# Kernel tuning notes

Hardware: AMD Instinct MI355X
Metric: run time of the kernel (lower is better)

The kernel has to match this reference:

```python
import jax, jax.numpy as jnp
import numpy as np

EMBED_DIM = 1024
HEADS = 16
HEAD_DIM = EMBED_DIM // HEADS
ROPE_THETA = 10000.0


def apply_rope(x):
    # x: [B, H, T, D]; standard rotary embedding on head_dim, half-split style
    D = x.shape[-1]
    T = x.shape[-2]
    half = D // 2
    inv_freq = 1.0 / (ROPE_THETA ** (jnp.arange(half, dtype=jnp.float32) / half))
    ang = jnp.arange(T, dtype=jnp.float32)[:, None] * inv_freq[None, :]  # [T, half]
    cos, sin = jnp.cos(ang), jnp.sin(ang)  # [T, half]
    x1, x2 = x[..., :half], x[..., half:]
    return jnp.concatenate([x1 * cos - x2 * sin, x1 * sin + x2 * cos], axis=-1)


def setup_inputs() -> dict:
    key = jax.random.key(0)
    ks = jax.random.split(key, 6)
    B, T, E, H = 2, 2048, EMBED_DIM, HEADS
    s = 0.02
    return {
        "x": jax.random.normal(ks[0], (B, T, E), dtype=jnp.float32),
        "w_qkv": jax.random.normal(ks[1], (E, 3 * E), dtype=jnp.float32) * s,
        "w_pre": jax.random.normal(ks[2], (H, H), dtype=jnp.float32) * s,
        "w_post": jax.random.normal(ks[3], (H, H), dtype=jnp.float32) * s,
        "w_out": jax.random.normal(ks[4], (E, E), dtype=jnp.float32) * s,
        "b_out": jax.random.normal(ks[5], (E,), dtype=jnp.float32) * s,
    }


def reference(x, w_qkv, w_pre, w_post, w_out, b_out):
    B, T, E = x.shape
    H, D = HEADS, HEAD_DIM
    qkv = x @ w_qkv  # [B, T, 3E]
    q, k, v = jnp.split(qkv, 3, axis=-1)
    q = q.reshape(B, T, H, D).transpose(0, 2, 1, 3)  # [B,H,T,D]
    k = k.reshape(B, T, H, D).transpose(0, 2, 1, 3)
    v = v.reshape(B, T, H, D).transpose(0, 2, 1, 3)
    q = apply_rope(q)
    k = apply_rope(k)
    scale = D ** -0.5
    dots = jnp.einsum('bhid,bhjd->bhij', q, k) * scale  # [B,H,T,T]
    # pre-softmax talking-heads mixing: new_head g = sum_h w_pre[g,h] * dots[h]
    dots = jnp.einsum('bhij,gh->bgij', dots, w_pre)
    attn = jax.nn.softmax(dots, axis=-1)
    # post-softmax mixing
    attn = jnp.einsum('bhij,gh->bgij', attn, w_post)
    out = jnp.einsum('bhij,bhjd->bhid', attn, v)  # [B,H,T,D]
    out = out.transpose(0, 2, 1, 3).reshape(B, T, E)
    return out @ w_out.T + b_out  # dropout is identity in eval
```

## Files before the change

kernel.cpp:

```cpp
#include <hip/hip_runtime.h>
#include <stdint.h>

typedef unsigned short u16;
typedef unsigned int   u32;

#define T_SEQ 2048
#define NB 2
#define NH 16
#define HD 64
#define E_DIM 1024
#define E3 3072
#define JS1 4
#define JS2 4
#define S2 36
#define OS2 1040

typedef float f32x4 __attribute__((ext_vector_type(4)));
typedef short s16x8 __attribute__((ext_vector_type(8)));

__device__ __forceinline__ float b2f(u16 u) {
    union { float f; u32 i; } v; v.i = ((u32)u) << 16; return v.f;
}
__device__ __forceinline__ u16 f2b(float f) {
    union { float f; u32 i; } v; v.f = f;
    u32 x = v.i;
    return (u16)((x + 0x7FFFu + ((x >> 16) & 1u)) >> 16);
}
__device__ __forceinline__ f32x4 mfma_bf16(s16x8 a, s16x8 b, f32x4 c) {
    return __builtin_amdgcn_mfma_f32_16x16x32_bf16(a, b, c, 0, 0, 0);
}
__device__ __forceinline__ void gl_lds16(const void* g, void* l) {
    __builtin_amdgcn_global_load_lds((const __attribute__((address_space(1))) void*)g,
                                     (__attribute__((address_space(3))) void*)l, 16, 0, 0);
}

__global__ void k_detect(const u16* __restrict__ x, int* __restrict__ flag) {
    __shared__ int cnt[256];
    int tid = threadIdx.x;
    int insane = 0;
    for (int i = tid; i < 4096; i += 256) {
        u16 v = x[2 * i];
        int e = (v >> 7) & 0xFF;
        if (e >= 143 || (e > 0 && e <= 100)) insane++;
    }
    cnt[tid] = insane;
    __syncthreads();
    if (tid == 0) {
        int s = 0;
        for (int k = 0; k < 256; ++k) s += cnt[k];
        *flag = (s > 512) ? 1 : 0;
    }
}

__global__ void k_cvt_bf16(const void* __restrict__ src, u16* __restrict__ dst,
                           int n, const int* __restrict__ flag) {
    int i = blockIdx.x * 256 + threadIdx.x;
    bool f32 = (*flag) != 0;
    if (i < n) dst[i] = f32 ? f2b(((const float*)src)[i]) : ((const u16*)src)[i];
}

__global__ void k_cvt_small(const void* __restrict__ a, const void* __restrict__ b,
                            const void* __restrict__ c, float* __restrict__ da,
                            float* __restrict__ db, float* __restrict__ dc,
                            const int* __restrict__ flag) {
    int i = blockIdx.x * 256 + threadIdx.x;
    bool f32 = (*flag) != 0;
    if (i < 256) {
        da[i] = f32 ? ((const float*)a)[i] : b2f(((const u16*)a)[i]);
    } else if (i < 512) {
        int j = i - 256;
        db[j] = f32 ? ((const float*)b)[j] : b2f(((const u16*)b)[j]);
    } else if (i < 1536) {
        int j = i - 512;
        dc[j] = f32 ? ((const float*)c)[j] : b2f(((const u16*)c)[j]);
    }
}

__global__ void k_transpose(const void* __restrict__ w, u16* __restrict__ wT,
                            const int* __restrict__ flag) {
    __shared__ u16 tile[32][33];
    bool f32 = (*flag) != 0;
    int n0 = blockIdx.x * 32;
    int k0 = blockIdx.y * 32;
    int tid = threadIdx.x;
    int c = tid & 31, r4 = tid >> 5;
#pragma unroll
    for (int it = 0; it < 4; ++it) {
        int r = r4 + it * 8;
        size_t idx = (size_t)(k0 + r) * E3 + n0 + c;
        tile[r][c] = f32 ? f2b(((const float*)w)[idx]) : ((const u16*)w)[idx];
    }
    __syncthreads();
#pragma unroll
    for (int it = 0; it < 4; ++it) {
        int r = r4 + it * 8;
        wT[(size_t)(n0 + r) * E_DIM + k0 + c] = tile[c][r];
    }
}

__global__ void k_qkv(const u16* __restrict__ A, const u16* __restrict__ Bm,
                      u16* __restrict__ C) {
    __shared__ __align__(16) u16 As[128 * 32];
    __shared__ __align__(16) u16 Bs[128 * 32];
    int m0 = blockIdx.x * 128, n0 = blockIdx.y * 128;
    int tid = threadIdx.x, lane = tid & 63, wv = tid >> 6;
    int q = lane >> 4, l = lane & 15;
    int wm = (wv >> 1) * 64, wn = (wv & 1) * 64;
    f32x4 acc[4][4] = {};
    int r16 = lane >> 2;
    int ccol = (lane & 3) * 8;
    for (int kc = 0; kc < 1024; kc += 32) {
#pragma unroll
        for (int j = 0; j < 4; ++j) {
            int chunk = wv * 4 + j;
            if (chunk < 8) {
                const u16* g = A + (size_t)(m0 + chunk * 16 + r16) * 1024 + kc + ccol;
                gl_lds16(g, (char*)As + chunk * 1024);
            } else {
                int ch = chunk - 8;
                const u16* g = Bm + (size_t)(n0 + ch * 16 + r16) * 1024 + kc + ccol;
                gl_lds16(g, (char*)Bs + ch * 1024);
            }
        }
        __syncthreads();
        s16x8 af[4], bf[4];
#pragma unroll
        for (int t = 0; t < 4; ++t) {
            af[t] = *(const s16x8*)(As + (wm + t * 16 + l) * 32 + q * 8);
            bf[t] = *(const s16x8*)(Bs + (wn + t * 16 + l) * 32 + q * 8);
        }
#pragma unroll
        for (int i = 0; i < 4; ++i)
#pragma unroll
            for (int j2 = 0; j2 < 4; ++j2)
                acc[i][j2] = mfma_bf16(af[i], bf[j2], acc[i][j2]);
        __syncthreads();
    }
#pragma unroll
    for (int i = 0; i < 4; ++i)
#pragma unroll
        for (int j2 = 0; j2 < 4; ++j2)
#pragma unroll
            for (int r = 0; r < 4; ++r) {
                int row = m0 + wm + i * 16 + q * 4 + r;
                int col = n0 + wn + j2 * 16 + l;
                C[(size_t)row * E3 + col] = f2b(acc[i][j2][r]);
            }
}

__global__ void k_rope(const u16* __restrict__ qkv, u16* __restrict__ qr,
                       u16* __restrict__ kr, u16* __restrict__ vt) {
    __shared__ u16 tile[64][66];
    int t0 = blockIdx.x * 64;
    int h = blockIdx.y, b = blockIdx.z;
    int tid = threadIdx.x;
    const float LN_TH = 9.210340371976184f / 32.0f;
    for (int src = 0; src < 3; ++src) {
        {
            int d = tid & 63, tr = tid >> 6;
#pragma unroll
            for (int it = 0; it < 16; ++it) {
                int t = tr + it * 4;
                tile[t][d] = qkv[(size_t)(b * T_SEQ + t0 + t) * E3 + src * E_DIM + h * HD + d];
            }
        }
        __syncthreads();
        if (src < 2) {
            u16* dst = (src == 0 ? qr : kr) + ((size_t)(b * NH + h) * T_SEQ) * HD;
            int d = tid & 31, tr = tid >> 5;
            float inv = __expf(-(float)d * LN_TH);
#pragma unroll
            for (int it = 0; it < 8; ++it) {
                int t = tr + it * 8;
                float ang = (float)(t0 + t) * inv;
                float sn, cs;
                __sincosf(ang, &sn, &cs);
                float x1 = b2f(tile[t][d]);
                float x2 = b2f(tile[t][d + 32]);
                dst[(size_t)(t0 + t) * HD + d]      = f2b(x1 * cs - x2 * sn);
                dst[(size_t)(t0 + t) * HD + d + 32] = f2b(x1 * sn + x2 * cs);
            }
        } else {
            int tl = tid & 63, dr = tid >> 6;
#pragma unroll
            for (int it = 0; it < 16; ++it) {
                int d = dr + it * 4;
                vt[((size_t)(b * NH + h) * HD + d) * T_SEQ + t0 + tl] = tile[tl][d];
            }
        }
        __syncthreads();
    }
}

__global__ __launch_bounds__(256, 3) void k_pass1(const u16* __restrict__ qr, const u16* __restrict__ kr,
                                                  const float* __restrict__ w_pre, float* __restrict__ lpart) {
    __shared__ __align__(16) u16 dotsb[2 * 256 * S2];
    int lin = blockIdx.x;
    int combo = lin & 7;
    int b = combo >> 2, js = combo & 3;
    int i0 = (lin >> 3) * 32;
    int tid = threadIdx.x, lane = tid & 63, wv = tid >> 6;
    int q = lane >> 4, l = lane & 15;
    {
        uint2 z = {0u, 0u};
        uint2* p0 = (uint2*)(dotsb + tid * S2 + 16);
        uint2* p1 = (uint2*)(dotsb + 256 * S2 + tid * S2 + 16);
        p0[0] = z; p0[1] = z; p0[2] = z; p0[3] = z;
        p1[0] = z; p1[1] = z; p1[2] = z; p1[3] = z;
    }
    s16x8 wpre;
#pragma unroll
    for (int jj = 0; jj < 8; ++jj) {
        int hh = q * 8 + jj;
        wpre[jj] = (hh < 16) ? (short)f2b(w_pre[l * 16 + hh] * 0.125f) : (short)0;
    }
    s16x8 qf[2][4][2];
#pragma unroll
    for (int it = 0; it < 2; ++it)
#pragma unroll
        for (int hl = 0; hl < 4; ++hl) {
            int h = wv * 4 + hl;
            const u16* ptr = qr + ((size_t)(b * NH + h) * T_SEQ + i0 + it * 16 + l) * HD + q * 8;
            qf[it][hl][0] = *(const s16x8*)(ptr);
            qf[it][hl][1] = *(const s16x8*)(ptr + 32);
        }
    float lacc[2][4][4] = {};
    __syncthreads();
    int jbase = js * (T_SEQ / JS1);
    for (int jstep = 0; jstep < (T_SEQ / JS1) / 16; ++jstep) {
        int jh = jbase + jstep * 16;
        s16x8 kf[4][2];
#pragma unroll
        for (int hl = 0; hl < 4; ++hl) {
            int h = wv * 4 + hl;
            const u16* ptr = kr + ((size_t)(b * NH + h) * T_SEQ + jh + l) * HD + q * 8;
            kf[hl][0] = *(const s16x8*)(ptr);
            kf[hl][1] = *(const s16x8*)(ptr + 32);
        }
#pragma unroll
        for (int it = 0; it < 2; ++it) {
            u16* dots = dotsb + (it & 1) * 256 * S2;
            f32x4 dacc[4];
#pragma unroll
            for (int hl = 0; hl < 4; ++hl) {
                f32x4 z = {};
                z = mfma_bf16(qf[it][hl][0], kf[hl][0], z);
                z = mfma_bf16(qf[it][hl][1], kf[hl][1], z);
                dacc[hl] = z;
            }
#pragma unroll
            for (int r = 0; r < 4; ++r) {
                int row = (q * 4 + r) * 16 + l;
                uint2 pk;
                pk.x = (u32)f2b(dacc[0][r]) | ((u32)f2b(dacc[1][r]) << 16);
                pk.y = (u32)f2b(dacc[2][r]) | ((u32)f2b(dacc[3][r]) << 16);
                *(uint2*)(dots + row * S2 + wv * 4) = pk;
            }
            __syncthreads();
#pragma unroll
            for (int cl = 0; cl < 4; ++cl) {
                int c = wv * 4 + cl;
                int rbase = (c * 16 + l) * S2;
                union { uint2 u2[2]; s16x8 v; } bf_;
                bf_.u2[0] = *(const uint2*)(dots + rbase + q * 8);
                bf_.u2[1] = *(const uint2*)(dots + rbase + q * 8 + 4);
                f32x4 s = {};
                s = mfma_bf16(wpre, bf_.v, s);
#pragma unroll
                for (int r = 0; r < 4; ++r)
                    lacc[it][cl][r] += __expf(fminf(s[r], 60.0f));
            }
        }
    }
#pragma unroll
    for (int it = 0; it < 2; ++it)
#pragma unroll
        for (int cl = 0; cl < 4; ++cl)
#pragma unroll
            for (int r = 0; r < 4; ++r) {
                float pv = lacc[it][cl][r];
                pv += __shfl_xor(pv, 1);
                pv += __shfl_xor(pv, 2);
                pv += __shfl_xor(pv, 4);
                pv += __shfl_xor(pv, 8);
                if (l == 0) {
                    int g = q * 4 + r;
                    int irow = wv * 4 + cl;
                    lpart[((size_t)(combo * NH + g)) * T_SEQ + i0 + it * 16 + irow] = pv;
                }
            }
}

__global__ __launch_bounds__(256, 2) void k_pass2(const u16* __restrict__ qr, const u16* __restrict__ kr,
                                                  const u16* __restrict__ vt, const float* __restrict__ lpart,
                                                  const float* __restrict__ w_pre, const float* __restrict__ w_post,
                                                  u16* __restrict__ opart) {
    __shared__ __align__(16) u16 smem[4 * 256 * S2];
    __shared__ float linv[2][16][16];
    u16* dotsb = smem;
    u16* aTb   = smem + 2 * 256 * S2;
    int lin = blockIdx.x;
    int combo = lin & 7;
    int b = combo >> 2, js = combo & 3;
    int i0 = (lin >> 3) * 32;
    int tid = threadIdx.x, lane = tid & 63, wv = tid >> 6;
    int q = lane >> 4, l = lane & 15;
    {
        uint2 z = {0u, 0u};
        uint2* p0 = (uint2*)(dotsb + tid * S2 + 16);
        uint2* p1 = (uint2*)(dotsb + 256 * S2 + tid * S2 + 16);
        p0[0] = z; p0[1] = z; p0[2] = z; p0[3] = z;
        p1[0] = z; p1[1] = z; p1[2] = z; p1[3] = z;
    }
    {
        int g = tid >> 4, il = tid & 15;
        float s0 = 0.f, s1 = 0.f;
#pragma unroll
        for (int j4 = 0; j4 < 4; ++j4) {
            const float* lp = lpart + ((size_t)((b * 4 + j4) * NH + g)) * T_SEQ + i0;
            s0 += lp[il];
            s1 += lp[16 + il];
        }
        linv[0][g][il] = 1.0f / s0;
        linv[1][g][il] = 1.0f / s1;
    }
    s16x8 wpre, wpost;
#pragma unroll
    for (int jj = 0; jj < 8; ++jj) {
        int hh = q * 8 + jj;
        wpre[jj]  = (hh < 16) ? (short)f2b(w_pre[l * 16 + hh] * 0.125f) : (short)0;
        wpost[jj] = (hh < 16) ? (short)f2b(w_post[l * 16 + hh]) : (short)0;
    }
    s16x8 qf[2][4][2];
#pragma unroll
    for (int it = 0; it < 2; ++it)
#pragma unroll
        for (int hl = 0; hl < 4; ++hl) {
            int h = wv * 4 + hl;
            const u16* ptr = qr + ((size_t)(b * NH + h) * T_SEQ + i0 + it * 16 + l) * HD + q * 8;
            qf[it][hl][0] = *(const s16x8*)(ptr);
            qf[it][hl][1] = *(const s16x8*)(ptr + 32);
        }
    f32x4 oacc[2][4][4] = {};
    __syncthreads();
    int jbase = js * (T_SEQ / JS2);
    for (int jst = 0; jst < (T_SEQ / JS2) / 32; ++jst) {
        int j0 = jbase + jst * 32;
#pragma unroll
        for (int jb = 0; jb < 2; ++jb) {
            int jh = j0 + jb * 16;
            s16x8 kf[4][2];
#pragma unroll
            for (int hl = 0; hl < 4; ++hl) {
                int h = wv * 4 + hl;
                const u16* ptr = kr + ((size_t)(b * NH + h) * T_SEQ + jh + l) * HD + q * 8;
                kf[hl][0] = *(const s16x8*)(ptr);
                kf[hl][1] = *(const s16x8*)(ptr + 32);
            }
#pragma unroll
            for (int it = 0; it < 2; ++it) {
                u16* dots = dotsb + ((jb * 2 + it) & 1) * 256 * S2;
                f32x4 dacc[4];
#pragma unroll
                for (int hl = 0; hl < 4; ++hl) {
                    f32x4 z = {};
                    z = mfma_bf16(qf[it][hl][0], kf[hl][0], z);
                    z = mfma_bf16(qf[it][hl][1], kf[hl][1], z);
                    dacc[hl] = z;
                }
#pragma unroll
                for (int r = 0; r < 4; ++r) {
                    int row = (q * 4 + r) * 16 + l;
                    uint2 pk;
                    pk.x = (u32)f2b(dacc[0][r]) | ((u32)f2b(dacc[1][r]) << 16);
                    pk.y = (u32)f2b(dacc[2][r]) | ((u32)f2b(dacc[3][r]) << 16);
                    *(uint2*)(dots + row * S2 + wv * 4) = pk;
                }
                __syncthreads();
                u16* aT = aTb + it * 256 * S2;
#pragma unroll
                for (int cl = 0; cl < 4; ++cl) {
                    int c = wv * 4 + cl;
                    int rbase = (c * 16 + l) * S2;
                    union { uint2 u2[2]; s16x8 v; } bf_;
                    bf_.u2[0] = *(const uint2*)(dots + rbase + q * 8);
                    bf_.u2[1] = *(const uint2*)(dots + rbase + q * 8 + 4);
                    f32x4 s = {};
                    s = mfma_bf16(wpre, bf_.v, s);
                    u32 pkx, pky;
                    {
                        u16 pu[4];
#pragma unroll
                        for (int r = 0; r < 4; ++r)
                            pu[r] = f2b(__expf(fminf(s[r], 60.0f)) * linv[it][q * 4 + r][c]);
                        pkx = (u32)pu[0] | ((u32)pu[1] << 16);
                        pky = (u32)pu[2] | ((u32)pu[3] << 16);
                    }
                    int srcA = (q & 1) * 32 + l;
                    int srcB = srcA + 16;
                    u32 x0 = (u32)__shfl((int)pkx, srcA);
                    u32 x1 = (u32)__shfl((int)pky, srcA);
                    u32 x2 = (u32)__shfl((int)pkx, srcB);
                    u32 x3 = (u32)__shfl((int)pky, srcB);
                    union { u32 u[4]; s16x8 v; } pf_;
                    bool hi = (q >= 2);
                    pf_.u[0] = hi ? 0u : x0;
                    pf_.u[1] = hi ? 0u : x1;
                    pf_.u[2] = hi ? 0u : x2;
                    pf_.u[3] = hi ? 0u : x3;
                    f32x4 a = {};
                    a = mfma_bf16(wpost, pf_.v, a);
#pragma unroll
                    for (int r = 0; r < 4; ++r)
                        aT[((q * 4 + r) * 16 + c) * S2 + jb * 16 + l] = f2b(a[r]);
                }
            }
        }
        __syncthreads();
#pragma unroll
        for (int gl = 0; gl < 4; ++gl) {
            int gp = wv * 4 + gl;
            int ar = (gp * 16 + l) * S2;
            union { uint2 u2[2]; s16x8 v; } af0, af1;
            af0.u2[0] = *(const uint2*)(aTb + ar + q * 8);
            af0.u2[1] = *(const uint2*)(aTb + ar + q * 8 + 4);
            af1.u2[0] = *(const uint2*)(aTb + 256 * S2 + ar + q * 8);
            af1.u2[1] = *(const uint2*)(aTb + 256 * S2 + ar + q * 8 + 4);
            const u16* vp = vt + ((size_t)(b * NH + gp) * HD) * T_SEQ + j0 + q * 8;
#pragma unroll
            for (int dt = 0; dt < 4; ++dt) {
                s16x8 bfrag = *(const s16x8*)(vp + (size_t)(dt * 16 + l) * T_SEQ);
                oacc[0][gl][dt] = mfma_bf16(af0.v, bfrag, oacc[0][gl][dt]);
                oacc[1][gl][dt] = mfma_bf16(af1.v, bfrag, oacc[1][gl][dt]);
            }
        }
    }
    size_t obase = (size_t)js * ((size_t)NB * T_SEQ * E_DIM);
#pragma unroll
    for (int it = 0; it < 2; ++it) {
        __syncthreads();
        u16* ostage = smem;
#pragma unroll
        for (int gl = 0; gl < 4; ++gl) {
            int gp = wv * 4 + gl;
#pragma unroll
            for (int dt = 0; dt < 4; ++dt)
#pragma unroll
                for (int r = 0; r < 4; ++r)
                    ostage[(q * 4 + r) * OS2 + gp * 64 + dt * 16 + l] = f2b(oacc[it][gl][dt][r]);
        }
        __syncthreads();
        int row = tid >> 4, sl = tid & 15;
        u16* gbase = opart + obase + ((size_t)(b * T_SEQ) + i0 + it * 16 + row) * E_DIM;
#pragma unroll
        for (int w = 0; w < 8; ++w) {
            uint4 v = *(const uint4*)(ostage + row * OS2 + w * 128 + sl * 8);
            *(uint4*)(gbase + w * 128 + sl * 8) = v;
        }
    }
}

__global__ void k_sum(const u16* __restrict__ op, u16* __restrict__ ab) {
    int i = (blockIdx.x * 256 + threadIdx.x) * 8;
    const size_t SZ = (size_t)4096 * 1024;
    union { uint4 v; u16 h[8]; } a0, a1, a2, a3, r;
    a0.v = *(const uint4*)(op + i);
    a1.v = *(const uint4*)(op + SZ + i);
    a2.v = *(const uint4*)(op + 2 * SZ + i);
    a3.v = *(const uint4*)(op + 3 * SZ + i);
#pragma unroll
    for (int k = 0; k < 8; ++k)
        r.h[k] = f2b(b2f(a0.h[k]) + b2f(a1.h[k]) + b2f(a2.h[k]) + b2f(a3.h[k]));
    *(uint4*)(ab + i) = r.v;
}

__global__ void k_outproj(const u16* __restrict__ A, const u16* __restrict__ Bm,
                          const float* __restrict__ bias, void* __restrict__ outv,
                          const int* __restrict__ flag) {
    __shared__ __align__(16) u16 As[128 * 32];
    __shared__ __align__(16) u16 Bs[128 * 32];
    bool f32 = (*flag) != 0;
    int m0 = blockIdx.x * 128, n0 = blockIdx.y * 128;
    int tid = threadIdx.x, lane = tid & 63, wv = tid >> 6;
    int q = lane >> 4, l = lane & 15;
    int wm = (wv >> 1) * 64, wn = (wv & 1) * 64;
    f32x4 acc[4][4] = {};
    int r16 = lane >> 2;
    int ccol = (lane & 3) * 8;
    for (int kc = 0; kc < 1024; kc += 32) {
#pragma unroll
        for (int j = 0; j < 4; ++j) {
            int chunk = wv * 4 + j;
            if (chunk < 8) {
                const u16* g = A + (size_t)(m0 + chunk * 16 + r16) * 1024 + kc + ccol;
                gl_lds16(g, (char*)As + chunk * 1024);
            } else {
                int ch = chunk - 8;
                const u16* g = Bm + (size_t)(n0 + ch * 16 + r16) * 1024 + kc + ccol;
                gl_lds16(g, (char*)Bs + ch * 1024);
            }
        }
        __syncthreads();
        s16x8 af[4], bf[4];
#pragma unroll
        for (int t = 0; t < 4; ++t) {
            af[t] = *(const s16x8*)(As + (wm + t * 16 + l) * 32 + q * 8);
            bf[t] = *(const s16x8*)(Bs + (wn + t * 16 + l) * 32 + q * 8);
        }
#pragma unroll
        for (int i = 0; i < 4; ++i)
#pragma unroll
            for (int j2 = 0; j2 < 4; ++j2)
                acc[i][j2] = mfma_bf16(af[i], bf[j2], acc[i][j2]);
        __syncthreads();
    }
#pragma unroll
    for (int i = 0; i < 4; ++i)
#pragma unroll
        for (int j2 = 0; j2 < 4; ++j2)
#pragma unroll
            for (int r = 0; r < 4; ++r) {
                int row = m0 + wm + i * 16 + q * 4 + r;
                int col = n0 + wn + j2 * 16 + l;
                float val = acc[i][j2][r] + bias[col];
                size_t idx = (size_t)row * E_DIM + col;
                if (f32) ((float*)outv)[idx] = val;
                else     ((u16*)outv)[idx]   = f2b(val);
            }
}

extern "C" void kernel_launch(void* const* d_in, const int* in_sizes, int n_in,
                              void* d_out, int out_size, void* d_ws, size_t ws_size,
                              hipStream_t stream) {
    (void)in_sizes; (void)n_in; (void)out_size; (void)ws_size;
    const void* x      = d_in[0];
    const void* w_qkv  = d_in[1];
    const void* w_pre  = d_in[2];
    const void* w_post = d_in[3];
    const void* w_out  = d_in[4];
    const void* b_out  = d_in[5];

    char* ws = (char*)d_ws;
    size_t off = 0;
    auto alloc = [&](size_t bytes) -> char* {
        char* p = ws + off;
        off += (bytes + 255) & ~(size_t)255;
        return p;
    };
    char* region0 = alloc((size_t)(8 + 6 + 24) * 1024 * 1024);
    u16*  xb      = (u16*)region0;
    u16*  wqkvT   = (u16*)(region0 + (size_t)8 * 1024 * 1024);
    u16*  qkv     = (u16*)(region0 + (size_t)14 * 1024 * 1024);
    u16*  opart   = (u16*)region0;
    int*  flag    = (int*)alloc(256);
    u16*  woutb   = (u16*)alloc((size_t)1024 * 1024 * 2);
    float* wpre_c = (float*)alloc(256 * 4);
    float* wpost_c= (float*)alloc(256 * 4);
    float* bout_c = (float*)alloc(1024 * 4);
    u16*  qr      = (u16*)alloc((size_t)NB * NH * T_SEQ * HD * 2);
    u16*  kr      = (u16*)alloc((size_t)NB * NH * T_SEQ * HD * 2);
    u16*  vt      = (u16*)alloc((size_t)NB * NH * HD * T_SEQ * 2);
    float* lpart  = (float*)alloc((size_t)8 * NH * T_SEQ * 4);
    u16*  ab      = (u16*)alloc((size_t)4096 * 1024 * 2);

    k_detect<<<1, 256, 0, stream>>>((const u16*)x, flag);
    k_cvt_bf16<<<16384, 256, 0, stream>>>(x, xb, 4096 * 1024, flag);
    k_cvt_bf16<<<4096, 256, 0, stream>>>(w_out, woutb, 1024 * 1024, flag);
    k_cvt_small<<<6, 256, 0, stream>>>(w_pre, w_post, b_out, wpre_c, wpost_c, bout_c, flag);
    k_transpose<<<dim3(96, 32), 256, 0, stream>>>(w_qkv, wqkvT, flag);
    k_qkv<<<dim3(32, 24), 256, 0, stream>>>(xb, wqkvT, qkv);
    k_rope<<<dim3(32, 16, 2), 256, 0, stream>>>(qkv, qr, kr, vt);
    k_pass1<<<512, 256, 0, stream>>>(qr, kr, wpre_c, lpart);
    k_pass2<<<512, 256, 0, stream>>>(qr, kr, vt, lpart, wpre_c, wpost_c, opart);
    k_sum<<<2048, 256, 0, stream>>>(opart, ab);
    k_outproj<<<dim3(32, 8), 256, 0, stream>>>(ab, woutb, bout_c, d_out, flag);
}
```

Baseline: 574.2 us.

## Use 16x16x16 fp16 MFMA for head mixing to drop padding and shuffles

The talking-heads pre- and post-softmax mixing steps now use a 16x16x16 fp16 MFMA instead of the 16x16x32 bf16 MFMA, which only used half of its K dimension. This removes the zero-padding of the dots buffer, the cross-lane shuffles that built the post-mix operand, and halves the dots LDS stride. Pass 2 also drops dots double-buffering and adds a barrier on each inner iteration, which frees LDS in exchange for more synchronisation. Storing dots as fp16 narrows their range compared with bf16.

```diff
diff --git a/kernel.cpp b/kernel.cpp
--- a/kernel.cpp
+++ b/kernel.cpp
@@ -12,11 +12,26 @@
 #define E3 3072
 #define JS1 4
 #define JS2 4
-#define S2 36
+#define S2A 36
 #define OS2 1040
+
+#if defined(__has_builtin)
+#if __has_builtin(__builtin_amdgcn_mfma_f32_16x16x16_f16)
+#define MIX16 1
+#endif
+#endif
+
+#ifdef MIX16
+#define S2D 18
+#else
+#define S2D 36
+#endif
 
 typedef float f32x4 __attribute__((ext_vector_type(4)));
 typedef short s16x8 __attribute__((ext_vector_type(8)));
+#ifdef MIX16
+typedef _Float16 f16x4 __attribute__((ext_vector_type(4)));
+#endif
 
 __device__ __forceinline__ float b2f(u16 u) {
     union { float f; u32 i; } v; v.i = ((u32)u) << 16; return v.f;
@@ -29,6 +44,11 @@
 __device__ __forceinline__ f32x4 mfma_bf16(s16x8 a, s16x8 b, f32x4 c) {
     return __builtin_amdgcn_mfma_f32_16x16x32_bf16(a, b, c, 0, 0, 0);
 }
+#ifdef MIX16
+__device__ __forceinline__ f32x4 mfma_f16_16(f16x4 a, f16x4 b, f32x4 c) {
+    return __builtin_amdgcn_mfma_f32_16x16x16_f16(a, b, c, 0, 0, 0);
+}
+#endif
 __device__ __forceinline__ void gl_lds16(const void* g, void* l) {
     __builtin_amdgcn_global_load_lds((const __attribute__((address_space(1))) void*)g,
                                      (__attribute__((address_space(3))) void*)l, 16, 0, 0);
@@ -194,26 +214,35 @@
 
 __global__ __launch_bounds__(256, 3) void k_pass1(const u16* __restrict__ qr, const u16* __restrict__ kr,
                                                   const float* __restrict__ w_pre, float* __restrict__ lpart) {
-    __shared__ __align__(16) u16 dotsb[2 * 256 * S2];
+    __shared__ __align__(16) u16 dotsb[2 * 256 * S2D];
     int lin = blockIdx.x;
     int combo = lin & 7;
     int b = combo >> 2, js = combo & 3;
     int i0 = (lin >> 3) * 32;
     int tid = threadIdx.x, lane = tid & 63, wv = tid >> 6;
     int q = lane >> 4, l = lane & 15;
+#ifndef MIX16
     {
         uint2 z = {0u, 0u};
-        uint2* p0 = (uint2*)(dotsb + tid * S2 + 16);
-        uint2* p1 = (uint2*)(dotsb + 256 * S2 + tid * S2 + 16);
+        uint2* p0 = (uint2*)(dotsb + tid * S2D + 16);
+        uint2* p1 = (uint2*)(dotsb + 256 * S2D + tid * S2D + 16);
         p0[0] = z; p0[1] = z; p0[2] = z; p0[3] = z;
         p1[0] = z; p1[1] = z; p1[2] = z; p1[3] = z;
     }
+#endif
+#ifdef MIX16
+    f16x4 wpre4;
+#pragma unroll
+    for (int jj = 0; jj < 4; ++jj)
+        wpre4[jj] = (_Float16)(w_pre[l * 16 + q * 4 + jj] * 0.125f);
+#else
     s16x8 wpre;
 #pragma unroll
     for (int jj = 0; jj < 8; ++jj) {
         int hh = q * 8 + jj;
         wpre[jj] = (hh < 16) ? (short)f2b(w_pre[l * 16 + hh] * 0.125f) : (short)0;
     }
+#endif
     s16x8 qf[2][4][2];
 #pragma unroll
     for (int it = 0; it < 2; ++it)
@@ -239,7 +268,7 @@
         }
 #pragma unroll
         for (int it = 0; it < 2; ++it) {
-            u16* dots = dotsb + (it & 1) * 256 * S2;
+            u16* dots = dotsb + (it & 1) * 256 * S2D;
             f32x4 dacc[4];
 #pragma unroll
             for (int hl = 0; hl < 4; ++hl) {
@@ -251,21 +280,38 @@
 #pragma unroll
             for (int r = 0; r < 4; ++r) {
                 int row = (q * 4 + r) * 16 + l;
+#ifdef MIX16
+                union { u32 u[2]; _Float16 h[4]; } pk;
+                pk.h[0] = (_Float16)dacc[0][r]; pk.h[1] = (_Float16)dacc[1][r];
+                pk.h[2] = (_Float16)dacc[2][r]; pk.h[3] = (_Float16)dacc[3][r];
+                u32* dw = (u32*)dots;
+                int wi = row * 9 + wv * 2;
+                dw[wi] = pk.u[0]; dw[wi + 1] = pk.u[1];
+#else
                 uint2 pk;
                 pk.x = (u32)f2b(dacc[0][r]) | ((u32)f2b(dacc[1][r]) << 16);
                 pk.y = (u32)f2b(dacc[2][r]) | ((u32)f2b(dacc[3][r]) << 16);
-                *(uint2*)(dots + row * S2 + wv * 4) = pk;
+                *(uint2*)(dots + row * S2D + wv * 4) = pk;
+#endif
             }
             __syncthreads();
 #pragma unroll
             for (int cl = 0; cl < 4; ++cl) {
                 int c = wv * 4 + cl;
-                int rbase = (c * 16 + l) * S2;
+                f32x4 s = {};
+#ifdef MIX16
+                const u32* dr_ = (const u32*)dots;
+                int ri = (c * 16 + l) * 9 + q * 2;
+                union { u32 u[2]; f16x4 v; } b4;
+                b4.u[0] = dr_[ri]; b4.u[1] = dr_[ri + 1];
+                s = mfma_f16_16(wpre4, b4.v, s);
+#else
+                int rbase = (c * 16 + l) * S2D;
                 union { uint2 u2[2]; s16x8 v; } bf_;
                 bf_.u2[0] = *(const uint2*)(dots + rbase + q * 8);
                 bf_.u2[1] = *(const uint2*)(dots + rbase + q * 8 + 4);
-                f32x4 s = {};
                 s = mfma_bf16(wpre, bf_.v, s);
+#endif
 #pragma unroll
                 for (int r = 0; r < 4; ++r)
                     lacc[it][cl][r] += __expf(fminf(s[r], 60.0f));
@@ -295,23 +341,23 @@
                                                   const u16* __restrict__ vt, const float* __restrict__ lpart,
                                                   const float* __restrict__ w_pre, const float* __restrict__ w_post,
                                                   u16* __restrict__ opart) {
-    __shared__ __align__(16) u16 smem[4 * 256 * S2];
+    __shared__ __align__(16) u16 smem[256 * S2D + 2 * 256 * S2A];
     __shared__ float linv[2][16][16];
-    u16* dotsb = smem;
-    u16* aTb   = smem + 2 * 256 * S2;
+    u16* dots = smem;
+    u16* aTb  = smem + 256 * S2D;
     int lin = blockIdx.x;
     int combo = lin & 7;
     int b = combo >> 2, js = combo & 3;
     int i0 = (lin >> 3) * 32;
     int tid = threadIdx.x, lane = tid & 63, wv = tid >> 6;
     int q = lane >> 4, l = lane & 15;
+#ifndef MIX16
     {
         uint2 z = {0u, 0u};
-        uint2* p0 = (uint2*)(dotsb + tid * S2 + 16);
-        uint2* p1 = (uint2*)(dotsb + 256 * S2 + tid * S2 + 16);
+        uint2* p0 = (uint2*)(dots + tid * S2D + 16);
         p0[0] = z; p0[1] = z; p0[2] = z; p0[3] = z;
-        p1[0] = z; p1[1] = z; p1[2] = z; p1[3] = z;
-    }
+    }
+#endif
     {
         int g = tid >> 4, il = tid & 15;
         float s0 = 0.f, s1 = 0.f;
@@ -324,6 +370,14 @@
         linv[0][g][il] = 1.0f / s0;
         linv[1][g][il] = 1.0f / s1;
     }
+#ifdef MIX16
+    f16x4 wpre4, wpost4;
+#pragma unroll
+    for (int jj = 0; jj < 4; ++jj) {
+        wpre4[jj]  = (_Float16)(w_pre[l * 16 + q * 4 + jj] * 0.125f);
+        wpost4[jj] = (_Float16)(w_post[l * 16 + q * 4 + jj]);
+    }
+#else
     s16x8 wpre, wpost;
 #pragma unroll
     for (int jj = 0; jj < 8; ++jj) {
@@ -331,6 +385,7 @@
         wpre[jj]  = (hh < 16) ? (short)f2b(w_pre[l * 16 + hh] * 0.125f) : (short)0;
         wpost[jj] = (hh < 16) ? (short)f2b(w_post[l * 16 + hh]) : (short)0;
     }
+#endif
     s16x8 qf[2][4][2];
 #pragma unroll
     for (int it = 0; it < 2; ++it)
@@ -359,7 +414,6 @@
             }
 #pragma unroll
             for (int it = 0; it < 2; ++it) {
-                u16* dots = dotsb + ((jb * 2 + it) & 1) * 256 * S2;
                 f32x4 dacc[4];
 #pragma unroll
                 for (int hl = 0; hl < 4; ++hl) {
@@ -371,21 +425,43 @@
 #pragma unroll
                 for (int r = 0; r < 4; ++r) {
                     int row = (q * 4 + r) * 16 + l;
+#ifdef MIX16
+                    union { u32 u[2]; _Float16 h[4]; } pk;
+                    pk.h[0] = (_Float16)dacc[0][r]; pk.h[1] = (_Float16)dacc[1][r];
+                    pk.h[2] = (_Float16)dacc[2][r]; pk.h[3] = (_Float16)dacc[3][r];
+                    u32* dw = (u32*)dots;
+                    int wi = row * 9 + wv * 2;
+                    dw[wi] = pk.u[0]; dw[wi + 1] = pk.u[1];
+#else
                     uint2 pk;
                     pk.x = (u32)f2b(dacc[0][r]) | ((u32)f2b(dacc[1][r]) << 16);
                     pk.y = (u32)f2b(dacc[2][r]) | ((u32)f2b(dacc[3][r]) << 16);
-                    *(uint2*)(dots + row * S2 + wv * 4) = pk;
+                    *(uint2*)(dots + row * S2D + wv * 4) = pk;
+#endif
                 }
                 __syncthreads();
-                u16* aT = aTb + it * 256 * S2;
+                u16* aT = aTb + it * 256 * S2A;
 #pragma unroll
                 for (int cl = 0; cl < 4; ++cl) {
                     int c = wv * 4 + cl;
-                    int rbase = (c * 16 + l) * S2;
+                    f32x4 s = {};
+#ifdef MIX16
+                    const u32* dr_ = (const u32*)dots;
+                    int ri = (c * 16 + l) * 9 + q * 2;
+                    union { u32 u[2]; f16x4 v; } b4;
+                    b4.u[0] = dr_[ri]; b4.u[1] = dr_[ri + 1];
+                    s = mfma_f16_16(wpre4, b4.v, s);
+                    f16x4 pf;
+#pragma unroll
+                    for (int r = 0; r < 4; ++r)
+                        pf[r] = (_Float16)(__expf(fminf(s[r], 60.0f)) * linv[it][q * 4 + r][c]);
+                    f32x4 a = {};
+                    a = mfma_f16_16(wpost4, pf, a);
+#else
+                    int rbase = (c * 16 + l) * S2D;
                     union { uint2 u2[2]; s16x8 v; } bf_;
                     bf_.u2[0] = *(const uint2*)(dots + rbase + q * 8);
                     bf_.u2[1] = *(const uint2*)(dots + rbase + q * 8 + 4);
-                    f32x4 s = {};
                     s = mfma_bf16(wpre, bf_.v, s);
                     u32 pkx, pky;
                     {
@@ -410,22 +486,23 @@
                     pf_.u[3] = hi ? 0u : x3;
                     f32x4 a = {};
                     a = mfma_bf16(wpost, pf_.v, a);
+#endif
 #pragma unroll
                     for (int r = 0; r < 4; ++r)
-                        aT[((q * 4 + r) * 16 + c) * S2 + jb * 16 + l] = f2b(a[r]);
+                        aT[((q * 4 + r) * 16 + c) * S2A + jb * 16 + l] = f2b(a[r]);
                 }
-            }
-        }
-        __syncthreads();
+                __syncthreads();
+            }
+        }
 #pragma unroll
         for (int gl = 0; gl < 4; ++gl) {
             int gp = wv * 4 + gl;
-            int ar = (gp * 16 + l) * S2;
+            int ar = (gp * 16 + l) * S2A;
             union { uint2 u2[2]; s16x8 v; } af0, af1;
             af0.u2[0] = *(const uint2*)(aTb + ar + q * 8);
             af0.u2[1] = *(const uint2*)(aTb + ar + q * 8 + 4);
-            af1.u2[0] = *(const uint2*)(aTb + 256 * S2 + ar + q * 8);
-            af1.u2[1] = *(const uint2*)(aTb + 256 * S2 + ar + q * 8 + 4);
+            af1.u2[0] = *(const uint2*)(aTb + 256 * S2A + ar + q * 8);
+            af1.u2[1] = *(const uint2*)(aTb + 256 * S2A + ar + q * 8 + 4);
             const u16* vp = vt + ((size_t)(b * NH + gp) * HD) * T_SEQ + j0 + q * 8;
 #pragma unroll
             for (int dt = 0; dt < 4; ++dt) {
```

New measurement: 527.4 us. 1.09x faster.
